# Kernel tuning notes

Hardware: AMD Instinct MI355X
Metric: run time of the kernel (lower is better)

Reference implementation:

```python
import jax, jax.numpy as jnp
import numpy as np

B, S, N, D = 4, 8, 1024, 512
PROJ_DIM = 512
HEADS = 4
EPSILON = 0.01


def pose_encoding(p):
    # p: [B,S,N,d]; faithful to PoseEncoding.__call__
    n, d = p.shape[-2], p.shape[-1]
    sin_d = d // 2 if d % 2 == 0 else (d - 1) // 2 + 1
    cos_d = d // 2 if d % 2 == 0 else (d - 1) // 2
    idx = jnp.arange(n, dtype=p.dtype)[:, None]
    ks = jnp.arange(sin_d, dtype=p.dtype)[None, :]
    kc = jnp.arange(cos_d, dtype=p.dtype)[None, :]
    sin_ape = jnp.sin(idx / (1000.0 * (2.0 * ks / d) + 0.01))  # [N, sin_d]
    cos_ape = jnp.cos(idx / (1000.0 * (2.0 * kc / d) + 0.01))  # [N, cos_d]
    pe = jnp.zeros((n, d), dtype=p.dtype)
    pe = pe.at[:, 0::2].set(sin_ape).at[:, 1::2].set(cos_ape)
    return p + pe


def setup_inputs() -> dict:
    key = jax.random.key(0)
    ks = jax.random.split(key, 5)
    x = jax.random.normal(ks[0], (B, S, N, D), dtype=jnp.float32)
    Wqkv = jax.random.normal(ks[1], (HEADS, D, 3 * D), dtype=jnp.float32) * 0.02
    bqkv = jax.random.normal(ks[2], (HEADS, 3 * D), dtype=jnp.float32) * 0.02
    Wp = jax.random.normal(ks[3], (HEADS, D, PROJ_DIM), dtype=jnp.float32) * 0.02
    bp = jax.random.normal(ks[4], (HEADS, PROJ_DIM), dtype=jnp.float32) * 0.02
    return {"x": x, "Wqkv": Wqkv, "bqkv": bqkv, "Wp": Wp, "bp": bp}


def reference(x, Wqkv, bqkv, Wp, bp):
    b, s, n, d = x.shape
    heads = Wqkv.shape[0]
    pred_proj = None
    proj = None
    for h in range(heads):  # small fixed loop over structurally distinct heads
        qkv = jax.nn.selu(jnp.einsum('bsnd,de->bsne', x, Wqkv[h]) + bqkv[h])
        qkv = qkv.reshape(b, s, n, 3, d)
        q, k, v = qkv[..., 0, :], qkv[..., 1, :], qkv[..., 2, :]
        # non-standard ordering: scale QK^T, multiply by V, THEN softmax
        qkT = jnp.einsum('bsnd,bsmd->bsnm', q, k) / d  # [B,S,N,N]
        att = jax.nn.softmax(jnp.einsum('bsnm,bsmd->bsnd', qkT, v), axis=-1)
        proj = jax.nn.gelu(jnp.einsum('bsnd,dp->bsnp', att, Wp[h]) + bp[h],
                           approximate=False)
        if pred_proj is None:
            pred_proj = proj
        else:
            proj = proj + EPSILON * pred_proj  # pred_proj stays = head-0 proj (as in source)
    return pose_encoding(proj)
```

## Files before the change

kernel.cpp:

```cpp
#include <hip/hip_runtime.h>
#include <hip/hip_bf16.h>
#include <math.h>

typedef unsigned short u16;
typedef unsigned int   u32;
typedef __bf16  v8bf  __attribute__((ext_vector_type(8)));
typedef float   v4f   __attribute__((ext_vector_type(4)));

#define EPS_H 0.01f

typedef const __attribute__((address_space(1))) void* gas_t;
typedef __attribute__((address_space(3))) void* las_t;
#define GL2LDS(g,l) __builtin_amdgcn_global_load_lds((gas_t)(const void*)(g), (las_t)(void*)(l), 16, 0, 0)

__device__ __forceinline__ u16 f2bf(float f) {
    __bf16 h = (__bf16)f;
    return *reinterpret_cast<u16*>(&h);
}
__device__ __forceinline__ float bfs(u16 v) { return __uint_as_float(((u32)v) << 16); }
__device__ __forceinline__ float selu_f(float x) {
    const float sc = 1.0507009873554805f, al = 1.6732632423543772f;
    return x > 0.f ? sc * x : sc * al * (__expf(x) - 1.0f);
}
__device__ __forceinline__ float gelu_f(float x) {
    return 0.5f * x * (1.f + erff(x * 0.7071067811865476f));
}
__device__ __forceinline__ float pe_val(int n, int j) {
    float t = 1000.0f * ((float)(j & ~1) * (1.0f / 512.0f)) + 0.01f;
    float a = (float)n / t;
    return (j & 1) ? cosf(a) : sinf(a);
}

__device__ __forceinline__ v8bf lfrag(const u16* base, int row, int lane) {
    int g = (lane >> 4) ^ ((row >> 1) & 3);
    return *(const v8bf*)((const char*)base + row * 64 + g * 16);
}

__device__ __forceinline__ void stage2(const u16* g, size_t gstride, u16* lds, int wave, int lane) {
    const int l2 = lane >> 2;
    #pragma unroll
    for (int i = 0; i < 4; ++i) {
        const int ib  = wave * 4 + i;
        const int sub = ib >> 3;
        const int rl  = (ib & 7) * 16 + l2;
        const int gs  = (lane & 3) ^ ((rl >> 1) & 3);
        GL2LDS((const char*)(g + (size_t)rl * gstride + sub * 32) + gs * 16,
               (char*)lds + ib * 1024);
    }
}

#define COMPUTE_TILE(Abuf, Bbuf)                                                   \
    {                                                                              \
        const u16* A0 = &(Abuf)[0];    const u16* A1 = &(Abuf)[4096];              \
        const u16* B0 = &(Bbuf)[0];    const u16* B1 = &(Bbuf)[4096];              \
        v8bf b0[4], b1[4];                                                         \
        _Pragma("unroll")                                                          \
        for (int fc = 0; fc < 4; ++fc) {                                           \
            const int brow = wn * 64 + fc * 16 + (lane & 15);                      \
            b0[fc] = lfrag(B0, brow, lane);                                        \
            b1[fc] = lfrag(B1, brow, lane);                                        \
        }                                                                          \
        __builtin_amdgcn_s_setprio(1);                                             \
        _Pragma("unroll")                                                          \
        for (int fr = 0; fr < 4; ++fr) {                                           \
            const int arow = wm * 64 + fr * 16 + (lane & 15);                      \
            v8bf a0 = lfrag(A0, arow, lane);                                       \
            v8bf a1 = lfrag(A1, arow, lane);                                       \
            _Pragma("unroll")                                                      \
            for (int fc = 0; fc < 4; ++fc) {                                       \
                acc[fr][fc] = __builtin_amdgcn_mfma_f32_16x16x32_bf16(a0, b0[fc], acc[fr][fc], 0, 0, 0); \
                acc[fr][fc] = __builtin_amdgcn_mfma_f32_16x16x32_bf16(a1, b1[fc], acc[fr][fc], 0, 0, 0); \
            }                                                                      \
        }                                                                          \
        __builtin_amdgcn_s_setprio(0);                                             \
    }

__global__ __launch_bounds__(256)
void k_xbf(const float* __restrict__ x, u16* __restrict__ xbf)
{
    const size_t i = ((size_t)blockIdx.x * 256 + threadIdx.x) * 8;
    float4 a = *(const float4*)&x[i];
    float4 b = *(const float4*)&x[i + 4];
    ushort4 o0, o1;
    o0.x = f2bf(a.x); o0.y = f2bf(a.y); o0.z = f2bf(a.z); o0.w = f2bf(a.w);
    o1.x = f2bf(b.x); o1.y = f2bf(b.y); o1.z = f2bf(b.z); o1.w = f2bf(b.w);
    *(ushort4*)&xbf[i] = o0;
    *(ushort4*)&xbf[i + 4] = o1;
}

__global__ __launch_bounds__(256, 1)
void k1_qkv(const u16* __restrict__ xbf, const u16* __restrict__ WT,
            const float* __restrict__ bias, u16* __restrict__ q,
            u16* __restrict__ kT, u16* __restrict__ vT)
{
    __shared__ u16 Als[2][8192];
    __shared__ u16 Bls[2][8192];
    const int tid = threadIdx.x, lane = tid & 63, wave = tid >> 6;
    const int orig = blockIdx.x + blockIdx.y * 12;
    const int swz  = (orig & 7) * 192 + (orig >> 3);
    const int col0 = (swz % 12) * 128, row0 = (swz / 12) * 128;
    const int wm = wave >> 1, wn = wave & 1;
    const u16* Ab = xbf + (size_t)row0 * 512;
    const u16* Bb = WT + (size_t)col0 * 512;
    v4f acc[4][4] = {};

    stage2(Ab, 512, &Als[0][0], wave, lane);
    stage2(Bb, 512, &Bls[0][0], wave, lane);
    for (int t = 0; t < 8; ++t) {
        const int c = t & 1;
        __syncthreads();
        if (t < 7) {
            const int k0 = (t + 1) * 64;
            stage2(Ab + k0, 512, &Als[c ^ 1][0], wave, lane);
            stage2(Bb + k0, 512, &Bls[c ^ 1][0], wave, lane);
        }
        COMPUTE_TILE(Als[c], Bls[c]);
    }

    const int region = col0 >> 9;
    #pragma unroll
    for (int fn = 0; fn < 4; ++fn) {
        const int c = col0 + wn * 64 + fn * 16 + (lane & 15);
        const float bc = bias[c];
        #pragma unroll
        for (int fm = 0; fm < 4; ++fm) {
            const int rb = row0 + wm * 64 + fm * 16 + ((lane >> 4) << 2);
            float v0 = selu_f(acc[fm][fn][0] + bc);
            float v1 = selu_f(acc[fm][fn][1] + bc);
            float v2 = selu_f(acc[fm][fn][2] + bc);
            float v3 = selu_f(acc[fm][fn][3] + bc);
            if (region == 0) {
                q[(size_t)(rb + 0) * 512 + c] = f2bf(v0);
                q[(size_t)(rb + 1) * 512 + c] = f2bf(v1);
                q[(size_t)(rb + 2) * 512 + c] = f2bf(v2);
                q[(size_t)(rb + 3) * 512 + c] = f2bf(v3);
            } else {
                ushort4 st; st.x = f2bf(v0); st.y = f2bf(v1); st.z = f2bf(v2); st.w = f2bf(v3);
                const int seq = rb >> 10, n = rb & 1023;
                u16* dst = (region == 1) ? kT : vT;
                const int cc = c - ((region == 1) ? 512 : 1024);
                *(ushort4*)&dst[(size_t)seq * 524288 + (size_t)cc * 1024 + n] = st;
            }
        }
    }
}

__global__ __launch_bounds__(256, 1)
void k2_ktv(const u16* __restrict__ kT, const u16* __restrict__ vT, u16* __restrict__ Mt)
{
    __shared__ u16 Als[2][8192];
    __shared__ u16 Bls[2][8192];
    const int tid = threadIdx.x, lane = tid & 63, wave = tid >> 6;
    const int d0 = blockIdx.x * 128, p0 = blockIdx.y * 128, seq = blockIdx.z;
    const u16* Ab = kT + (size_t)seq * 524288 + (size_t)d0 * 1024;
    const u16* Bb = vT + (size_t)seq * 524288 + (size_t)p0 * 1024;
    const int wm = wave >> 1, wn = wave & 1;
    v4f acc[4][4] = {};

    stage2(Ab, 1024, &Als[0][0], wave, lane);
    stage2(Bb, 1024, &Bls[0][0], wave, lane);
    for (int t = 0; t < 16; ++t) {
        const int c = t & 1;
        __syncthreads();
        if (t < 15) {
            const int m0 = (t + 1) * 64;
            stage2(Ab + m0, 1024, &Als[c ^ 1][0], wave, lane);
            stage2(Bb + m0, 1024, &Bls[c ^ 1][0], wave, lane);
        }
        COMPUTE_TILE(Als[c], Bls[c]);
    }

    #pragma unroll
    for (int fn = 0; fn < 4; ++fn) {
        const int p = p0 + wn * 64 + fn * 16 + (lane & 15);
        #pragma unroll
        for (int fm = 0; fm < 4; ++fm) {
            const int d = d0 + wm * 64 + fm * 16 + ((lane >> 4) << 2);
            ushort4 st;
            st.x = f2bf(acc[fm][fn][0] * (1.f / 512.f));
            st.y = f2bf(acc[fm][fn][1] * (1.f / 512.f));
            st.z = f2bf(acc[fm][fn][2] * (1.f / 512.f));
            st.w = f2bf(acc[fm][fn][3] * (1.f / 512.f));
            *(ushort4*)&Mt[(size_t)seq * 262144 + (size_t)p * 512 + d] = st;
        }
    }
}

__global__ __launch_bounds__(256, 1)
void k3a_s(const u16* __restrict__ q, const u16* __restrict__ Mt, u16* __restrict__ S)
{
    __shared__ u16 Als[2][8192];
    __shared__ u16 Bls[2][8192];
    const int tid = threadIdx.x, lane = tid & 63, wave = tid >> 6;
    const int orig = blockIdx.x + blockIdx.y * 4;
    const int swz  = (orig & 7) * 64 + (orig >> 3);
    const int p0 = (swz % 4) * 128, row0 = (swz / 4) * 128;
    const int seq = row0 >> 10;
    const u16* Ab = q + (size_t)row0 * 512;
    const u16* Bb = Mt + (size_t)seq * 262144 + (size_t)p0 * 512;
    const int wm = wave >> 1, wn = wave & 1;
    v4f acc[4][4] = {};

    stage2(Ab, 512, &Als[0][0], wave, lane);
    stage2(Bb, 512, &Bls[0][0], wave, lane);
    for (int t = 0; t < 8; ++t) {
        const int c = t & 1;
        __syncthreads();
        if (t < 7) {
            const int k0 = (t + 1) * 64;
            stage2(Ab + k0, 512, &Als[c ^ 1][0], wave, lane);
            stage2(Bb + k0, 512, &Bls[c ^ 1][0], wave, lane);
        }
        COMPUTE_TILE(Als[c], Bls[c]);
    }

    #pragma unroll
    for (int fn = 0; fn < 4; ++fn) {
        const int c = p0 + wn * 64 + fn * 16 + (lane & 15);
        #pragma unroll
        for (int fm = 0; fm < 4; ++fm) {
            const int rb = row0 + wm * 64 + fm * 16 + ((lane >> 4) << 2);
            S[(size_t)(rb + 0) * 512 + c] = f2bf(acc[fm][fn][0]);
            S[(size_t)(rb + 1) * 512 + c] = f2bf(acc[fm][fn][1]);
            S[(size_t)(rb + 2) * 512 + c] = f2bf(acc[fm][fn][2]);
            S[(size_t)(rb + 3) * 512 + c] = f2bf(acc[fm][fn][3]);
        }
    }
}

__global__ __launch_bounds__(256)
void k3b_sm(u16* __restrict__ S)
{
    const int row  = blockIdx.x * 4 + (threadIdx.x >> 6);
    const int lane = threadIdx.x & 63;
    u16* rp = S + (size_t)row * 512 + lane * 8;
    ushort4 u0 = *(const ushort4*)rp;
    ushort4 u1 = *(const ushort4*)(rp + 4);
    float f[8] = {bfs(u0.x), bfs(u0.y), bfs(u0.z), bfs(u0.w),
                  bfs(u1.x), bfs(u1.y), bfs(u1.z), bfs(u1.w)};
    float m = f[0];
    #pragma unroll
    for (int j = 1; j < 8; ++j) m = fmaxf(m, f[j]);
    #pragma unroll
    for (int off = 32; off > 0; off >>= 1) m = fmaxf(m, __shfl_xor(m, off));
    float s = 0.f;
    #pragma unroll
    for (int j = 0; j < 8; ++j) { f[j] = __expf(f[j] - m); s += f[j]; }
    #pragma unroll
    for (int off = 32; off > 0; off >>= 1) s += __shfl_xor(s, off);
    const float inv = 1.0f / s;
    ushort4 o0, o1;
    o0.x = f2bf(f[0] * inv); o0.y = f2bf(f[1] * inv);
    o0.z = f2bf(f[2] * inv); o0.w = f2bf(f[3] * inv);
    o1.x = f2bf(f[4] * inv); o1.y = f2bf(f[5] * inv);
    o1.z = f2bf(f[6] * inv); o1.w = f2bf(f[7] * inv);
    *(ushort4*)rp = o0;
    *(ushort4*)(rp + 4) = o1;
}

__global__ __launch_bounds__(256, 1)
void k3c_proj(const u16* __restrict__ att, const u16* __restrict__ WpT,
              const float* __restrict__ bp, const float* __restrict__ pe,
              float* __restrict__ out, const int mode, const int rowbase)
{
    __shared__ u16 Als[2][8192];
    __shared__ u16 Bls[2][8192];
    const int tid = threadIdx.x, lane = tid & 63, wave = tid >> 6;
    const int orig = blockIdx.x + blockIdx.y * 4;
    const int swz  = (orig & 7) * 64 + (orig >> 3);
    const int e0 = (swz % 4) * 128, row0 = (swz / 4) * 128;
    const u16* Ab = att + (size_t)row0 * 512;
    const u16* Bb = WpT + (size_t)e0 * 512;
    const int wm = wave >> 1, wn = wave & 1;
    v4f acc[4][4] = {};

    stage2(Ab, 512, &Als[0][0], wave, lane);
    stage2(Bb, 512, &Bls[0][0], wave, lane);
    for (int t = 0; t < 8; ++t) {
        const int c = t & 1;
        __syncthreads();
        if (t < 7) {
            const int k0 = (t + 1) * 64;
            stage2(Ab + k0, 512, &Als[c ^ 1][0], wave, lane);
            stage2(Bb + k0, 512, &Bls[c ^ 1][0], wave, lane);
        }
        COMPUTE_TILE(Als[c], Bls[c]);
    }

    #pragma unroll
    for (int fn = 0; fn < 4; ++fn) {
        const int e = e0 + wn * 64 + fn * 16 + (lane & 15);
        const float be = bp[e];
        #pragma unroll
        for (int fm = 0; fm < 4; ++fm) {
            const int rb = row0 + wm * 64 + fm * 16 + ((lane >> 4) << 2);
            #pragma unroll
            for (int j = 0; j < 4; ++j) {
                const int r = rowbase + rb + j;
                const float g = gelu_f(acc[fm][fn][j] + be);
                const size_t o = (size_t)r * 512 + e;
                if (mode == 0) out[o] = g;
                else           out[o] = g + EPS_H * out[o] + pe[(r & 1023) * 512 + e];
            }
        }
    }
}

__global__ __launch_bounds__(256)
void k_tr(const float* __restrict__ src, u16* __restrict__ dst, int rows, int cols)
{
    __shared__ float t[32][33];
    const int tid = threadIdx.x;
    const int c0 = blockIdx.x * 32, r0 = blockIdx.y * 32;
    #pragma unroll
    for (int i = 0; i < 4; ++i) {
        int idx = tid + i * 256;
        int rr = idx >> 5, cc = idx & 31;
        t[rr][cc] = src[(size_t)(r0 + rr) * cols + c0 + cc];
    }
    __syncthreads();
    #pragma unroll
    for (int i = 0; i < 4; ++i) {
        int idx = tid + i * 256;
        int rr = idx >> 5, cc = idx & 31;
        dst[(size_t)(c0 + rr) * rows + r0 + cc] = f2bf(t[cc][rr]);
    }
}

__global__ __launch_bounds__(256)
void k_pe(float* __restrict__ pe)
{
    int idx = blockIdx.x * 256 + threadIdx.x;
    pe[idx] = pe_val(idx >> 9, idx & 511);
}

extern "C" void kernel_launch(void* const* d_in, const int* in_sizes, int n_in,
                              void* d_out, int out_size, void* d_ws, size_t ws_size,
                              hipStream_t stream)
{
    const float* x    = (const float*)d_in[0];
    const float* Wqkv = (const float*)d_in[1];
    const float* bqkv = (const float*)d_in[2];
    const float* Wp   = (const float*)d_in[3];
    const float* bp   = (const float*)d_in[4];
    float* out = (float*)d_out;

    char* ws = (char*)d_ws;
    u16*   xbf = (u16*)(ws);
    u16*   q   = (u16*)(ws + 33554432);
    u16*   kT  = (u16*)(ws + 50331648);
    u16*   vT  = (u16*)(ws + 67108864);
    u16*   Mt  = (u16*)(ws + 83886080);
    u16*   WqT = (u16*)(ws + 92274688);
    u16*   WpT = (u16*)(ws + 95420416);
    float* pe  = (float*)(ws + 96468992);
    u16*   S   = kT;

    k_xbf<<<8192, 256, 0, stream>>>(x, xbf);
    k_pe<<<2048, 256, 0, stream>>>(pe);
    for (int hh = 0; hh < 2; ++hh) {
        const int h = hh ? 3 : 0;
        k_tr<<<dim3(48, 16), 256, 0, stream>>>(Wqkv + (size_t)h * 786432, WqT + (size_t)hh * 786432, 512, 1536);
        k_tr<<<dim3(16, 16), 256, 0, stream>>>(Wp   + (size_t)h * 262144, WpT + (size_t)hh * 262144, 512, 512);
    }
    for (int p = 0; p < 2; ++p) {
        const int h = p ? 3 : 0;
        for (int ck = 0; ck < 2; ++ck) {
            const u16* xc = xbf + (size_t)ck * 16384 * 512;
            k1_qkv<<<dim3(12, 128), 256, 0, stream>>>(xc, WqT + (size_t)p * 786432,
                                                      bqkv + (size_t)h * 1536, q, kT, vT);
            k2_ktv<<<dim3(4, 4, 16), 256, 0, stream>>>(kT, vT, Mt);
            k3a_s<<<dim3(4, 128), 256, 0, stream>>>(q, Mt, S);
            k3b_sm<<<4096, 256, 0, stream>>>(S);
            k3c_proj<<<dim3(4, 128), 256, 0, stream>>>(S, WpT + (size_t)p * 262144,
                                                       bp + (size_t)h * 512, pe, out, p, ck * 16384);
        }
    }
}
```

Baseline: 459.4 us.

## Use 256x256 tiles for QKV GEMM and deepen prefetch in all GEMMs

Replaces the 128x128 QKV projection kernel with a 512-thread, 256x256-tile version using 128KB dynamic LDS and its own swizzled staging. It also switches the QKV, K^T V, S and projection GEMMs from load-ahead-by-one to load-ahead-by-two. Completion is tracked with explicit vmcnt waits and barriers instead of __syncthreads. The goal is more data reuse per tile and better hiding of global-to-LDS latency. The risks are fewer blocks for the QKV GEMM, higher register pressure from 32 accumulators, and fragile hand-written wait counts.

```diff
diff --git a/kernel.cpp b/kernel.cpp
--- a/kernel.cpp
+++ b/kernel.cpp
@@ -12,6 +12,11 @@
 typedef const __attribute__((address_space(1))) void* gas_t;
 typedef __attribute__((address_space(3))) void* las_t;
 #define GL2LDS(g,l) __builtin_amdgcn_global_load_lds((gas_t)(const void*)(g), (las_t)(void*)(l), 16, 0, 0)
+
+#define VMW8()   asm volatile("s_waitcnt vmcnt(8)" ::: "memory")
+#define VMW0()   asm volatile("s_waitcnt vmcnt(0)" ::: "memory")
+#define BAR()    __builtin_amdgcn_s_barrier()
+#define SCHED0() __builtin_amdgcn_sched_barrier(0)
 
 __device__ __forceinline__ u16 f2bf(float f) {
     __bf16 h = (__bf16)f;
@@ -88,33 +93,73 @@
     *(ushort4*)&xbf[i + 4] = o1;
 }
 
-__global__ __launch_bounds__(256, 1)
-void k1_qkv(const u16* __restrict__ xbf, const u16* __restrict__ WT,
-            const float* __restrict__ bias, u16* __restrict__ q,
-            u16* __restrict__ kT, u16* __restrict__ vT)
-{
-    __shared__ u16 Als[2][8192];
-    __shared__ u16 Bls[2][8192];
+__global__ __launch_bounds__(512, 2)
+void k1_qkv256(const u16* __restrict__ xbf, const u16* __restrict__ WT,
+               const float* __restrict__ bias, u16* __restrict__ q,
+               u16* __restrict__ kT, u16* __restrict__ vT)
+{
+    extern __shared__ u16 lds[];
     const int tid = threadIdx.x, lane = tid & 63, wave = tid >> 6;
-    const int orig = blockIdx.x + blockIdx.y * 12;
-    const int swz  = (orig & 7) * 192 + (orig >> 3);
-    const int col0 = (swz % 12) * 128, row0 = (swz / 12) * 128;
-    const int wm = wave >> 1, wn = wave & 1;
-    const u16* Ab = xbf + (size_t)row0 * 512;
-    const u16* Bb = WT + (size_t)col0 * 512;
-    v4f acc[4][4] = {};
-
-    stage2(Ab, 512, &Als[0][0], wave, lane);
-    stage2(Bb, 512, &Bls[0][0], wave, lane);
+    const int orig = blockIdx.x + blockIdx.y * 6;
+    const int swz  = (orig & 7) * 48 + (orig >> 3);
+    const int col0 = (swz % 6) * 256, row0 = (swz / 6) * 256;
+    const int wm = wave >> 2, wn = wave & 3;
+    const u16* Ag = xbf + (size_t)row0 * 512;
+    const u16* Bg = WT + (size_t)col0 * 512;
+    v4f acc[8][4] = {};
+
+    auto stg = [&](const u16* g, u16* dst, int k0) {
+        const int l2 = lane >> 2;
+        #pragma unroll
+        for (int i = 0; i < 4; ++i) {
+            const int ib = wave * 4 + i;
+            const int s  = ib >> 3;
+            const int rl = (ib & 7) * 16 + l2;
+            const int row = (s >> 1) * 128 + rl;
+            const int gs = (lane & 3) ^ ((rl >> 1) & 3);
+            GL2LDS((const char*)(g + (size_t)row * 512 + k0 + (s & 1) * 32) + gs * 16,
+                   (char*)dst + ib * 1024);
+        }
+    };
+
+    stg(Ag, lds, 0);          stg(Bg, lds + 32768, 0);
+    stg(Ag, lds + 16384, 64); stg(Bg, lds + 49152, 64);
+
     for (int t = 0; t < 8; ++t) {
         const int c = t & 1;
-        __syncthreads();
-        if (t < 7) {
-            const int k0 = (t + 1) * 64;
-            stage2(Ab + k0, 512, &Als[c ^ 1][0], wave, lane);
-            stage2(Bb + k0, 512, &Bls[c ^ 1][0], wave, lane);
-        }
-        COMPUTE_TILE(Als[c], Bls[c]);
+        if (t < 7) VMW8(); else VMW0();
+        BAR(); SCHED0();
+        {
+            const u16* Ac = lds + c * 16384;
+            const u16* Bc = lds + 32768 + c * 16384;
+            v8bf bf[4][2];
+            #pragma unroll
+            for (int fn = 0; fn < 4; ++fn) {
+                const int bsub = (wn >> 1) * 2;
+                const int brow = (wn & 1) * 64 + fn * 16 + (lane & 15);
+                bf[fn][0] = lfrag(Bc + (bsub + 0) * 4096, brow, lane);
+                bf[fn][1] = lfrag(Bc + (bsub + 1) * 4096, brow, lane);
+            }
+            __builtin_amdgcn_s_setprio(1);
+            #pragma unroll
+            for (int fm = 0; fm < 8; ++fm) {
+                const int asub = wm * 2;
+                const int arow = fm * 16 + (lane & 15);
+                v8bf a0 = lfrag(Ac + (asub + 0) * 4096, arow, lane);
+                v8bf a1 = lfrag(Ac + (asub + 1) * 4096, arow, lane);
+                #pragma unroll
+                for (int fn = 0; fn < 4; ++fn) {
+                    acc[fm][fn] = __builtin_amdgcn_mfma_f32_16x16x32_bf16(a0, bf[fn][0], acc[fm][fn], 0, 0, 0);
+                    acc[fm][fn] = __builtin_amdgcn_mfma_f32_16x16x32_bf16(a1, bf[fn][1], acc[fm][fn], 0, 0, 0);
+                }
+            }
+            __builtin_amdgcn_s_setprio(0);
+        }
+        BAR(); SCHED0();
+        if (t + 2 < 8) {
+            stg(Ag, lds + c * 16384, (t + 2) * 64);
+            stg(Bg, lds + 32768 + c * 16384, (t + 2) * 64);
+        }
     }
 
     const int region = col0 >> 9;
@@ -123,8 +168,8 @@
         const int c = col0 + wn * 64 + fn * 16 + (lane & 15);
         const float bc = bias[c];
         #pragma unroll
-        for (int fm = 0; fm < 4; ++fm) {
-            const int rb = row0 + wm * 64 + fm * 16 + ((lane >> 4) << 2);
+        for (int fm = 0; fm < 8; ++fm) {
+            const int rb = row0 + wm * 128 + fm * 16 + ((lane >> 4) << 2);
             float v0 = selu_f(acc[fm][fn][0] + bc);
             float v1 = selu_f(acc[fm][fn][1] + bc);
             float v2 = selu_f(acc[fm][fn][2] + bc);
@@ -157,17 +202,21 @@
     const int wm = wave >> 1, wn = wave & 1;
     v4f acc[4][4] = {};
 
-    stage2(Ab, 1024, &Als[0][0], wave, lane);
-    stage2(Bb, 1024, &Bls[0][0], wave, lane);
+    stage2(Ab,      1024, &Als[0][0], wave, lane);
+    stage2(Bb,      1024, &Bls[0][0], wave, lane);
+    stage2(Ab + 64, 1024, &Als[1][0], wave, lane);
+    stage2(Bb + 64, 1024, &Bls[1][0], wave, lane);
     for (int t = 0; t < 16; ++t) {
         const int c = t & 1;
-        __syncthreads();
-        if (t < 15) {
-            const int m0 = (t + 1) * 64;
-            stage2(Ab + m0, 1024, &Als[c ^ 1][0], wave, lane);
-            stage2(Bb + m0, 1024, &Bls[c ^ 1][0], wave, lane);
-        }
+        if (t < 15) VMW8(); else VMW0();
+        BAR(); SCHED0();
         COMPUTE_TILE(Als[c], Bls[c]);
+        BAR(); SCHED0();
+        if (t + 2 < 16) {
+            const int m0 = (t + 2) * 64;
+            stage2(Ab + m0, 1024, &Als[c][0], wave, lane);
+            stage2(Bb + m0, 1024, &Bls[c][0], wave, lane);
+        }
     }
 
     #pragma unroll
@@ -201,17 +250,21 @@
     const int wm = wave >> 1, wn = wave & 1;
     v4f acc[4][4] = {};
 
-    stage2(Ab, 512, &Als[0][0], wave, lane);
-    stage2(Bb, 512, &Bls[0][0], wave, lane);
+    stage2(Ab,      512, &Als[0][0], wave, lane);
+    stage2(Bb,      512, &Bls[0][0], wave, lane);
+    stage2(Ab + 64, 512, &Als[1][0], wave, lane);
+    stage2(Bb + 64, 512, &Bls[1][0], wave, lane);
     for (int t = 0; t < 8; ++t) {
         const int c = t & 1;
-        __syncthreads();
-        if (t < 7) {
-            const int k0 = (t + 1) * 64;
-            stage2(Ab + k0, 512, &Als[c ^ 1][0], wave, lane);
-            stage2(Bb + k0, 512, &Bls[c ^ 1][0], wave, lane);
-        }
+        if (t < 7) VMW8(); else VMW0();
+        BAR(); SCHED0();
         COMPUTE_TILE(Als[c], Bls[c]);
+        BAR(); SCHED0();
+        if (t + 2 < 8) {
+            const int k0 = (t + 2) * 64;
+            stage2(Ab + k0, 512, &Als[c][0], wave, lane);
+            stage2(Bb + k0, 512, &Bls[c][0], wave, lane);
+        }
     }
 
     #pragma unroll
@@ -274,17 +327,21 @@
     const int wm = wave >> 1, wn = wave & 1;
     v4f acc[4][4] = {};
 
-    stage2(Ab, 512, &Als[0][0], wave, lane);
-    stage2(Bb, 512, &Bls[0][0], wave, lane);
+    stage2(Ab,      512, &Als[0][0], wave, lane);
+    stage2(Bb,      512, &Bls[0][0], wave, lane);
+    stage2(Ab + 64, 512, &Als[1][0], wave, lane);
+    stage2(Bb + 64, 512, &Bls[1][0], wave, lane);
     for (int t = 0; t < 8; ++t) {
         const int c = t & 1;
-        __syncthreads();
-        if (t < 7) {
-            const int k0 = (t + 1) * 64;
-            stage2(Ab + k0, 512, &Als[c ^ 1][0], wave, lane);
-            stage2(Bb + k0, 512, &Bls[c ^ 1][0], wave, lane);
-        }
+        if (t < 7) VMW8(); else VMW0();
+        BAR(); SCHED0();
         COMPUTE_TILE(Als[c], Bls[c]);
+        BAR(); SCHED0();
+        if (t + 2 < 8) {
+            const int k0 = (t + 2) * 64;
+            stage2(Ab + k0, 512, &Als[c][0], wave, lane);
+            stage2(Bb + k0, 512, &Bls[c][0], wave, lane);
+        }
     }
 
     #pragma unroll
@@ -356,6 +413,9 @@
     float* pe  = (float*)(ws + 96468992);
     u16*   S   = kT;
 
+    (void)hipFuncSetAttribute((const void*)k1_qkv256,
+                              hipFuncAttributeMaxDynamicSharedMemorySize, 131072);
+
     k_xbf<<<8192, 256, 0, stream>>>(x, xbf);
     k_pe<<<2048, 256, 0, stream>>>(pe);
     for (int hh = 0; hh < 2; ++hh) {
@@ -367,8 +427,8 @@
         const int h = p ? 3 : 0;
         for (int ck = 0; ck < 2; ++ck) {
             const u16* xc = xbf + (size_t)ck * 16384 * 512;
-            k1_qkv<<<dim3(12, 128), 256, 0, stream>>>(xc, WqT + (size_t)p * 786432,
-                                                      bqkv + (size_t)h * 1536, q, kT, vT);
+            k1_qkv256<<<dim3(6, 64), 512, 131072, stream>>>(xc, WqT + (size_t)p * 786432,
+                                                            bqkv + (size_t)h * 1536, q, kT, vT);
             k2_ktv<<<dim3(4, 4, 16), 256, 0, stream>>>(kT, vT, Mt);
             k3a_s<<<dim3(4, 128), 256, 0, stream>>>(q, Mt, S);
             k3b_sm<<<4096, 256, 0, stream>>>(S);
```

New measurement: 476.0 us. +3.6%, slower.
